# Kernel optimization log

Hardware: AMD Instinct MI355X
Metric: run time of the kernel (lower is better)

Reference implementation:

```python
import jax, jax.numpy as jnp
import numpy as np

N_NEIGHBORS = 3


def square_distance(src, dst):
    # src: [B,N,3], dst: [B,M,3] -> [B,N,M]
    d = -2.0 * jnp.einsum('bnc,bmc->bnm', src, dst)
    d = d + jnp.sum(src * src, axis=-1)[:, :, None]
    d = d + jnp.sum(dst * dst, axis=-1)[:, None, :]
    return d


def setup_inputs() -> dict:
    key = jax.random.key(0)
    k1, k2, k3 = jax.random.split(key, 3)
    B, N_q, N_k, C = 4, 8192, 2048, 128
    xyz_q = jax.random.normal(k1, (B, N_q, 3), dtype=jnp.float32)
    xyz_k = jax.random.normal(k2, (B, N_k, 3), dtype=jnp.float32)
    v_k = jax.random.normal(k3, (B, N_k, C), dtype=jnp.float32)
    return {"xyz_q": xyz_q, "xyz_k": xyz_k, "v_k": v_k}


def reference(xyz_q, xyz_k, v_k):
    # pairwise squared distances [B,N_q,N_k]
    sqrdists = square_distance(xyz_q, xyz_k)
    # kNN: smallest nsample distances per query
    neg_dist, idx = jax.lax.top_k(-sqrdists, N_NEIGHBORS)  # [B,N_q,k]
    dist_nearest = jnp.take_along_axis(sqrdists, idx, axis=2)
    dist_nearest = jnp.maximum(dist_nearest, 1e-10)
    weights = 1.0 / dist_nearest
    weights = weights / jnp.sum(weights, axis=-1, keepdims=True)
    # gather neighbor features: [B,N_q,k,C]
    grouped_v = jax.vmap(lambda v, i: v[i])(v_k, idx)
    # inverse-distance-weighted interpolation
    v_q = jnp.einsum('bnk,bnkc->bnc', weights, grouped_v)
    return v_q
```

## Files before the change

### kernel.cpp

```cpp
#include <hip/hip_runtime.h>
#include <cfloat>

#define BB 4
#define NQ 8192
#define NK 2048
#define CC 128
#define C4 (CC / 4)

#define QPB 64
#define SPLITS 16
#define KPS (NK / SPLITS)
#define NTHR (QPB * SPLITS)

__global__ __launch_bounds__(NTHR, 8) void fp_fused(
    const float*  __restrict__ xyz_q,
    const float*  __restrict__ xyz_k,
    const float4* __restrict__ vk,
    float4*       __restrict__ out)
{
    __shared__ float4 ks[NK];
    __shared__ unsigned long long rd[NTHR][4];
    __shared__ float sw[QPB][4];
    __shared__ int   si[QPB][4];

    const int b     = blockIdx.y;
    const int qbase = blockIdx.x * QPB;
    const int tid   = threadIdx.x;
    const int lane  = tid & 63;
    const int split = tid >> 6;
    const int q     = qbase + lane;

    {
        const float* kb = xyz_k + (size_t)b * NK * 3;
        #pragma unroll
        for (int i = tid; i < NK; i += NTHR) {
            ks[i] = make_float4(kb[i * 3 + 0], kb[i * 3 + 1], kb[i * 3 + 2], 0.0f);
        }
    }

    const float qx = xyz_q[(b * NQ + q) * 3 + 0];
    const float qy = xyz_q[(b * NQ + q) * 3 + 1];
    const float qz = xyz_q[(b * NQ + q) * 3 + 2];

    __syncthreads();

    const int kbeg = __builtin_amdgcn_readfirstlane(split * KPS);

    float u0 = FLT_MAX, u1 = FLT_MAX, u2 = FLT_MAX, u3 = FLT_MAX;

    #pragma unroll 8
    for (int j = 0; j < KPS; ++j) {
        float4 kk = ks[kbeg + j];
        float dx = qx - kk.x, dy = qy - kk.y, dz = qz - kk.z;
        float t = fmaf(dx, dx, fmaf(dy, dy, dz * dz));
        float p = __uint_as_float((__float_as_uint(t) & 0xFFFFFF80u) | (unsigned)j);
        u3 = __builtin_amdgcn_fmed3f(p, u2, u3);
        u2 = __builtin_amdgcn_fmed3f(p, u1, u2);
        u1 = __builtin_amdgcn_fmed3f(p, u0, u1);
        u0 = fminf(u0, p);
    }

    {
        float uu[4] = { u0, u1, u2, u3 };
        #pragma unroll
        for (int c = 0; c < 4; ++c) {
            int kidx = kbeg + (int)(__float_as_uint(uu[c]) & 0x7Fu);
            float4 ka = ks[kidx];
            double dx = (double)qx - (double)ka.x;
            double dy = (double)qy - (double)ka.y;
            double dz = (double)qz - (double)ka.z;
            double dd = dx * dx + dy * dy + dz * dz;
            unsigned long long pk =
                (((unsigned long long)__double_as_longlong(dd)) & ~0x7FFull)
                | (unsigned long long)kidx;
            rd[tid][c] = pk;
        }
    }
    __syncthreads();

    if (tid < QPB) {
        double m0 = DBL_MAX, m1 = DBL_MAX, m2 = DBL_MAX;
        #pragma unroll 4
        for (int s = 0; s < SPLITS; ++s) {
            #pragma unroll
            for (int c = 0; c < 4; ++c) {
                double x = __longlong_as_double((long long)rd[s * QPB + lane][c]);
                double a1 = fmax(x, m1), a0 = fmax(x, m0);
                m2 = fmin(m2, a1);
                m1 = fmin(m1, a0);
                m0 = fmin(m0, x);
            }
        }
        unsigned long long b0 = (unsigned long long)__double_as_longlong(m0);
        unsigned long long b1 = (unsigned long long)__double_as_longlong(m1);
        unsigned long long b2 = (unsigned long long)__double_as_longlong(m2);
        double e0 = __longlong_as_double((long long)(b0 & ~0x7FFull));
        double e1 = __longlong_as_double((long long)(b1 & ~0x7FFull));
        double e2 = __longlong_as_double((long long)(b2 & ~0x7FFull));
        e0 = fmax(e0, 1e-10);
        e1 = fmax(e1, 1e-10);
        e2 = fmax(e2, 1e-10);
        double w0 = 1.0 / e0, w1 = 1.0 / e1, w2 = 1.0 / e2;
        double s  = w0 + w1 + w2;
        sw[lane][0] = (float)(w0 / s);
        sw[lane][1] = (float)(w1 / s);
        sw[lane][2] = (float)(w2 / s);
        si[lane][0] = (int)(b0 & 0x7FFull);
        si[lane][1] = (int)(b1 & 0x7FFull);
        si[lane][2] = (int)(b2 & 0x7FFull);
    }
    __syncthreads();

    const float4* vb = vk + (size_t)b * NK * C4;
    float4* ob = out + ((size_t)b * NQ + qbase) * C4;
    #pragma unroll
    for (int r = 0; r < (QPB * C4) / NTHR; ++r) {
        int o  = r * NTHR + tid;
        int qq = o >> 5;
        int c4 = o & (C4 - 1);
        float w0 = sw[qq][0], w1 = sw[qq][1], w2 = sw[qq][2];
        int   j0 = si[qq][0], j1 = si[qq][1], j2 = si[qq][2];
        float4 v0 = vb[j0 * C4 + c4];
        float4 v1 = vb[j1 * C4 + c4];
        float4 v2 = vb[j2 * C4 + c4];
        float4 res;
        res.x = fmaf(w0, v0.x, fmaf(w1, v1.x, w2 * v2.x));
        res.y = fmaf(w0, v0.y, fmaf(w1, v1.y, w2 * v2.y));
        res.z = fmaf(w0, v0.z, fmaf(w1, v1.z, w2 * v2.z));
        res.w = fmaf(w0, v0.w, fmaf(w1, v1.w, w2 * v2.w));
        ob[o] = res;
    }
}

extern "C" void kernel_launch(void* const* d_in, const int* in_sizes, int n_in,
                              void* d_out, int out_size, void* d_ws, size_t ws_size,
                              hipStream_t stream)
{
    const float* xyz_q = (const float*)d_in[0];
    const float* xyz_k = (const float*)d_in[1];
    const float* v_k   = (const float*)d_in[2];

    fp_fused<<<dim3(NQ / QPB, BB), dim3(NTHR), 0, stream>>>(
        xyz_q, xyz_k, (const float4*)v_k, (float4*)d_out);
}
```

Measured before the change: 89.20 us.

## Stream keys via scalar loads from a prepacked global buffer instead of LDS

Adds a pre-pass kernel that packs key coordinates with their squared norm into float4 in the workspace. The main kernel drops the LDS key staging and its barrier, and reads 4 keys per iteration with wave-uniform s_load_dwordx16 into SGPRs. The distance is computed in expanded form (q^2 + k^2 - 2q·k, with a small offset added). This aims to remove LDS read traffic and cut per-key VALU work. The risks are a serialising lgkmcnt wait each iteration with unroll 1, an extra kernel launch, and the expanded-form distance reordering near-ties before the double-precision refinement.

Result: slower. 92.87 us (+4.1%).

```diff
diff --git a/kernel.cpp b/kernel.cpp
--- a/kernel.cpp
+++ b/kernel.cpp
@@ -12,13 +12,26 @@
 #define KPS (NK / SPLITS)
 #define NTHR (QPB * SPLITS)
 
-__global__ __launch_bounds__(NTHR, 8) void fp_fused(
+typedef float sfvec __attribute__((ext_vector_type(16)));
+
+__global__ __launch_bounds__(256) void pack_keys(
+    const float* __restrict__ xyz_k, float4* __restrict__ keys)
+{
+    int i = blockIdx.x * 256 + threadIdx.x;
+    if (i < BB * NK) {
+        float x = xyz_k[i * 3 + 0];
+        float y = xyz_k[i * 3 + 1];
+        float z = xyz_k[i * 3 + 2];
+        keys[i] = make_float4(x, y, z, fmaf(x, x, fmaf(y, y, z * z)));
+    }
+}
+
+__global__ __launch_bounds__(NTHR, 8) void fp_main(
     const float*  __restrict__ xyz_q,
-    const float*  __restrict__ xyz_k,
+    const float4* __restrict__ keys,
     const float4* __restrict__ vk,
     float4*       __restrict__ out)
 {
-    __shared__ float4 ks[NK];
     __shared__ unsigned long long rd[NTHR][4];
     __shared__ float sw[QPB][4];
     __shared__ int   si[QPB][4];
@@ -30,42 +43,46 @@
     const int split = tid >> 6;
     const int q     = qbase + lane;
 
-    {
-        const float* kb = xyz_k + (size_t)b * NK * 3;
+    const float qx = xyz_q[(b * NQ + q) * 3 + 0];
+    const float qy = xyz_q[(b * NQ + q) * 3 + 1];
+    const float qz = xyz_q[(b * NQ + q) * 3 + 2];
+    const float qq = fmaf(qx, qx, fmaf(qy, qy, qz * qz)) + 1.0e-3f;
+    const float ax = -2.0f * qx, ay = -2.0f * qy, az = -2.0f * qz;
+
+    const int kbeg = __builtin_amdgcn_readfirstlane(split * KPS);
+    const sfvec* kp4 = (const sfvec*)(keys + (size_t)b * NK + kbeg);
+
+    float u0 = FLT_MAX, u1 = FLT_MAX, u2 = FLT_MAX, u3 = FLT_MAX;
+
+    #pragma unroll 1
+    for (int jb = 0; jb < KPS / 4; ++jb) {
+        const sfvec* addr = kp4 + jb;
+        sfvec kk;
+        asm("s_load_dwordx16 %0, %1, 0x0" : "=s"(kk) : "s"(addr));
+        asm("s_waitcnt lgkmcnt(0)" : "+s"(kk));
         #pragma unroll
-        for (int i = tid; i < NK; i += NTHR) {
-            ks[i] = make_float4(kb[i * 3 + 0], kb[i * 3 + 1], kb[i * 3 + 2], 0.0f);
+        for (int c = 0; c < 4; ++c) {
+            float kx = kk[c * 4 + 0];
+            float ky = kk[c * 4 + 1];
+            float kz = kk[c * 4 + 2];
+            float kw = kk[c * 4 + 3];
+            float t = fmaf(ax, kx, fmaf(ay, ky, fmaf(az, kz, qq))) + kw;
+            float p = __uint_as_float((__float_as_uint(t) & 0xFFFFFF80u)
+                                      | (unsigned)(jb * 4 + c));
+            u3 = __builtin_amdgcn_fmed3f(p, u2, u3);
+            u2 = __builtin_amdgcn_fmed3f(p, u1, u2);
+            u1 = __builtin_amdgcn_fmed3f(p, u0, u1);
+            u0 = fminf(u0, p);
         }
     }
 
-    const float qx = xyz_q[(b * NQ + q) * 3 + 0];
-    const float qy = xyz_q[(b * NQ + q) * 3 + 1];
-    const float qz = xyz_q[(b * NQ + q) * 3 + 2];
-
-    __syncthreads();
-
-    const int kbeg = __builtin_amdgcn_readfirstlane(split * KPS);
-
-    float u0 = FLT_MAX, u1 = FLT_MAX, u2 = FLT_MAX, u3 = FLT_MAX;
-
-    #pragma unroll 8
-    for (int j = 0; j < KPS; ++j) {
-        float4 kk = ks[kbeg + j];
-        float dx = qx - kk.x, dy = qy - kk.y, dz = qz - kk.z;
-        float t = fmaf(dx, dx, fmaf(dy, dy, dz * dz));
-        float p = __uint_as_float((__float_as_uint(t) & 0xFFFFFF80u) | (unsigned)j);
-        u3 = __builtin_amdgcn_fmed3f(p, u2, u3);
-        u2 = __builtin_amdgcn_fmed3f(p, u1, u2);
-        u1 = __builtin_amdgcn_fmed3f(p, u0, u1);
-        u0 = fminf(u0, p);
-    }
-
     {
+        const float4* kg = keys + (size_t)b * NK;
         float uu[4] = { u0, u1, u2, u3 };
         #pragma unroll
         for (int c = 0; c < 4; ++c) {
             int kidx = kbeg + (int)(__float_as_uint(uu[c]) & 0x7Fu);
-            float4 ka = ks[kidx];
+            float4 ka = kg[kidx];
             double dx = (double)qx - (double)ka.x;
             double dy = (double)qy - (double)ka.y;
             double dz = (double)qz - (double)ka.z;
@@ -116,10 +133,10 @@
     #pragma unroll
     for (int r = 0; r < (QPB * C4) / NTHR; ++r) {
         int o  = r * NTHR + tid;
-        int qq = o >> 5;
+        int qq2 = o >> 5;
         int c4 = o & (C4 - 1);
-        float w0 = sw[qq][0], w1 = sw[qq][1], w2 = sw[qq][2];
-        int   j0 = si[qq][0], j1 = si[qq][1], j2 = si[qq][2];
+        float w0 = sw[qq2][0], w1 = sw[qq2][1], w2 = sw[qq2][2];
+        int   j0 = si[qq2][0], j1 = si[qq2][1], j2 = si[qq2][2];
         float4 v0 = vb[j0 * C4 + c4];
         float4 v1 = vb[j1 * C4 + c4];
         float4 v2 = vb[j2 * C4 + c4];
@@ -140,6 +157,9 @@
     const float* xyz_k = (const float*)d_in[1];
     const float* v_k   = (const float*)d_in[2];
 
-    fp_fused<<<dim3(NQ / QPB, BB), dim3(NTHR), 0, stream>>>(
-        xyz_q, xyz_k, (const float4*)v_k, (float4*)d_out);
+    float4* keys = (float4*)d_ws;
+
+    pack_keys<<<dim3((BB * NK + 255) / 256), dim3(256), 0, stream>>>(xyz_k, keys);
+    fp_main<<<dim3(NQ / QPB, BB), dim3(NTHR), 0, stream>>>(
+        xyz_q, keys, (const float4*)v_k, (float4*)d_out);
 }
```

## Expand distance algebraically, process four queries per thread, prepack keys

Applied to the files above, without the earlier changes.

A new pre-kernel packs the key coordinates plus their squared norm into float4 in workspace. The main kernel computes distance as q·(-2k)+|q|²+|k|², which cuts per-pair arithmetic. Each thread now handles four queries, so one shared-memory key load is reused across them and the thread count drops to 256. The fp32 scan keeps top-4 per split with an 11-bit index packed into the low mantissa bits. Merging keeps top-8 candidates that are re-ranked in double precision, which adds a second launch and a more approximate fp32 pre-filter in exchange.

New measurement: 90.23 us. About the same (+1.1%).

```diff
diff --git a/kernel.cpp b/kernel.cpp
--- a/kernel.cpp
+++ b/kernel.cpp
@@ -10,90 +10,137 @@
 #define QPB 64
 #define SPLITS 16
 #define KPS (NK / SPLITS)
-#define NTHR (QPB * SPLITS)
+#define QPT 4
+#define NTHR (QPB * SPLITS / QPT)
+#define RD_ROW 68
 
-__global__ __launch_bounds__(NTHR, 8) void fp_fused(
+static __device__ __forceinline__ float fmed3(float a, float b, float c) {
+    return __builtin_amdgcn_fmed3f(a, b, c);
+}
+
+__global__ __launch_bounds__(256) void pack_keys(
+    const float* __restrict__ xyz_k, float4* __restrict__ keys)
+{
+    int i = blockIdx.x * 256 + threadIdx.x;
+    if (i < BB * NK) {
+        float x = xyz_k[i * 3 + 0];
+        float y = xyz_k[i * 3 + 1];
+        float z = xyz_k[i * 3 + 2];
+        keys[i] = make_float4(x, y, z, fmaf(x, x, fmaf(y, y, z * z)));
+    }
+}
+
+__global__ __launch_bounds__(NTHR, 2) void fp_main(
     const float*  __restrict__ xyz_q,
-    const float*  __restrict__ xyz_k,
+    const float4* __restrict__ keys,
     const float4* __restrict__ vk,
     float4*       __restrict__ out)
 {
-    __shared__ float4 ks[NK];
-    __shared__ unsigned long long rd[NTHR][4];
-    __shared__ float sw[QPB][4];
-    __shared__ int   si[QPB][4];
+    __shared__ float4  ks[NK];
+    __shared__ unsigned rd[QPB][RD_ROW];
+    __shared__ float   sw[QPB][4];
+    __shared__ int     si[QPB][4];
 
     const int b     = blockIdx.y;
     const int qbase = blockIdx.x * QPB;
     const int tid   = threadIdx.x;
-    const int lane  = tid & 63;
-    const int split = tid >> 6;
-    const int q     = qbase + lane;
+    const int split = tid >> 4;
+    const int g     = tid & 15;
 
-    {
-        const float* kb = xyz_k + (size_t)b * NK * 3;
-        #pragma unroll
-        for (int i = tid; i < NK; i += NTHR) {
-            ks[i] = make_float4(kb[i * 3 + 0], kb[i * 3 + 1], kb[i * 3 + 2], 0.0f);
-        }
+    #pragma unroll
+    for (int i = tid; i < NK; i += NTHR) ks[i] = keys[(size_t)b * NK + i];
+
+    float ax[QPT], ay[QPT], az[QPT], qb_[QPT];
+    #pragma unroll
+    for (int qi = 0; qi < QPT; ++qi) {
+        int q = qbase + g + 16 * qi;
+        float qx = xyz_q[(b * NQ + q) * 3 + 0];
+        float qy = xyz_q[(b * NQ + q) * 3 + 1];
+        float qz = xyz_q[(b * NQ + q) * 3 + 2];
+        ax[qi] = -2.0f * qx; ay[qi] = -2.0f * qy; az[qi] = -2.0f * qz;
+        qb_[qi] = fmaf(qx, qx, fmaf(qy, qy, qz * qz)) + 1.0e-3f;
     }
-
-    const float qx = xyz_q[(b * NQ + q) * 3 + 0];
-    const float qy = xyz_q[(b * NQ + q) * 3 + 1];
-    const float qz = xyz_q[(b * NQ + q) * 3 + 2];
-
     __syncthreads();
 
-    const int kbeg = __builtin_amdgcn_readfirstlane(split * KPS);
+    const int kbeg = split * KPS;
 
-    float u0 = FLT_MAX, u1 = FLT_MAX, u2 = FLT_MAX, u3 = FLT_MAX;
+    float u[QPT][4];
+    #pragma unroll
+    for (int qi = 0; qi < QPT; ++qi)
+        u[qi][0] = u[qi][1] = u[qi][2] = u[qi][3] = FLT_MAX;
 
     #pragma unroll 8
     for (int j = 0; j < KPS; ++j) {
         float4 kk = ks[kbeg + j];
-        float dx = qx - kk.x, dy = qy - kk.y, dz = qz - kk.z;
-        float t = fmaf(dx, dx, fmaf(dy, dy, dz * dz));
-        float p = __uint_as_float((__float_as_uint(t) & 0xFFFFFF80u) | (unsigned)j);
-        u3 = __builtin_amdgcn_fmed3f(p, u2, u3);
-        u2 = __builtin_amdgcn_fmed3f(p, u1, u2);
-        u1 = __builtin_amdgcn_fmed3f(p, u0, u1);
-        u0 = fminf(u0, p);
+        unsigned kidx = (unsigned)(kbeg + j);
+        #pragma unroll
+        for (int qi = 0; qi < QPT; ++qi) {
+            float t = fmaf(ax[qi], kk.x,
+                      fmaf(ay[qi], kk.y,
+                      fmaf(az[qi], kk.z, qb_[qi]))) + kk.w;
+            float p = __uint_as_float((__float_as_uint(t) & 0xFFFFF800u) | kidx);
+            u[qi][3] = fmed3(p, u[qi][2], u[qi][3]);
+            u[qi][2] = fmed3(p, u[qi][1], u[qi][2]);
+            u[qi][1] = fmed3(p, u[qi][0], u[qi][1]);
+            u[qi][0] = fminf(u[qi][0], p);
+        }
     }
 
-    {
-        float uu[4] = { u0, u1, u2, u3 };
-        #pragma unroll
-        for (int c = 0; c < 4; ++c) {
-            int kidx = kbeg + (int)(__float_as_uint(uu[c]) & 0x7Fu);
-            float4 ka = ks[kidx];
-            double dx = (double)qx - (double)ka.x;
-            double dy = (double)qy - (double)ka.y;
-            double dz = (double)qz - (double)ka.z;
-            double dd = dx * dx + dy * dy + dz * dz;
-            unsigned long long pk =
-                (((unsigned long long)__double_as_longlong(dd)) & ~0x7FFull)
-                | (unsigned long long)kidx;
-            rd[tid][c] = pk;
-        }
+    #pragma unroll
+    for (int qi = 0; qi < QPT; ++qi) {
+        int ql = g + 16 * qi;
+        uint4 v = make_uint4(__float_as_uint(u[qi][0]), __float_as_uint(u[qi][1]),
+                             __float_as_uint(u[qi][2]), __float_as_uint(u[qi][3]));
+        *(uint4*)&rd[ql][split * 4] = v;
     }
     __syncthreads();
 
     if (tid < QPB) {
-        double m0 = DBL_MAX, m1 = DBL_MAX, m2 = DBL_MAX;
+        const int ql = tid;
+        float m[8];
+        #pragma unroll
+        for (int c = 0; c < 8; ++c) m[c] = FLT_MAX;
         #pragma unroll 4
-        for (int s = 0; s < SPLITS; ++s) {
+        for (int i = 0; i < SPLITS; ++i) {
+            uint4 v = *(const uint4*)&rd[ql][i * 4];
+            unsigned vv[4] = { v.x, v.y, v.z, v.w };
             #pragma unroll
             for (int c = 0; c < 4; ++c) {
-                double x = __longlong_as_double((long long)rd[s * QPB + lane][c]);
-                double a1 = fmax(x, m1), a0 = fmax(x, m0);
-                m2 = fmin(m2, a1);
-                m1 = fmin(m1, a0);
-                m0 = fmin(m0, x);
+                float p = __uint_as_float(vv[c]);
+                m[7] = fmed3(p, m[6], m[7]);
+                m[6] = fmed3(p, m[5], m[6]);
+                m[5] = fmed3(p, m[4], m[5]);
+                m[4] = fmed3(p, m[3], m[4]);
+                m[3] = fmed3(p, m[2], m[3]);
+                m[2] = fmed3(p, m[1], m[2]);
+                m[1] = fmed3(p, m[0], m[1]);
+                m[0] = fminf(m[0], p);
             }
         }
-        unsigned long long b0 = (unsigned long long)__double_as_longlong(m0);
-        unsigned long long b1 = (unsigned long long)__double_as_longlong(m1);
-        unsigned long long b2 = (unsigned long long)__double_as_longlong(m2);
+        int q = qbase + ql;
+        double qx = (double)xyz_q[(b * NQ + q) * 3 + 0];
+        double qy = (double)xyz_q[(b * NQ + q) * 3 + 1];
+        double qz = (double)xyz_q[(b * NQ + q) * 3 + 2];
+        double M0 = DBL_MAX, M1 = DBL_MAX, M2 = DBL_MAX;
+        #pragma unroll
+        for (int c = 0; c < 8; ++c) {
+            unsigned ki = __float_as_uint(m[c]) & 0x7FFu;
+            float4 ka = ks[ki];
+            double dx = qx - (double)ka.x;
+            double dy = qy - (double)ka.y;
+            double dz = qz - (double)ka.z;
+            double dd = dx * dx + dy * dy + dz * dz;
+            double x = __longlong_as_double(
+                (long long)((((unsigned long long)__double_as_longlong(dd)) & ~0x7FFull)
+                            | (unsigned long long)ki));
+            double a1 = fmax(x, M1), a0 = fmax(x, M0);
+            M2 = fmin(M2, a1);
+            M1 = fmin(M1, a0);
+            M0 = fmin(M0, x);
+        }
+        unsigned long long b0 = (unsigned long long)__double_as_longlong(M0);
+        unsigned long long b1 = (unsigned long long)__double_as_longlong(M1);
+        unsigned long long b2 = (unsigned long long)__double_as_longlong(M2);
         double e0 = __longlong_as_double((long long)(b0 & ~0x7FFull));
         double e1 = __longlong_as_double((long long)(b1 & ~0x7FFull));
         double e2 = __longlong_as_double((long long)(b2 & ~0x7FFull));
@@ -102,12 +149,12 @@
         e2 = fmax(e2, 1e-10);
         double w0 = 1.0 / e0, w1 = 1.0 / e1, w2 = 1.0 / e2;
         double s  = w0 + w1 + w2;
-        sw[lane][0] = (float)(w0 / s);
-        sw[lane][1] = (float)(w1 / s);
-        sw[lane][2] = (float)(w2 / s);
-        si[lane][0] = (int)(b0 & 0x7FFull);
-        si[lane][1] = (int)(b1 & 0x7FFull);
-        si[lane][2] = (int)(b2 & 0x7FFull);
+        sw[ql][0] = (float)(w0 / s);
+        sw[ql][1] = (float)(w1 / s);
+        sw[ql][2] = (float)(w2 / s);
+        si[ql][0] = (int)(b0 & 0x7FFull);
+        si[ql][1] = (int)(b1 & 0x7FFull);
+        si[ql][2] = (int)(b2 & 0x7FFull);
     }
     __syncthreads();
 
@@ -140,6 +187,9 @@
     const float* xyz_k = (const float*)d_in[1];
     const float* v_k   = (const float*)d_in[2];
 
-    fp_fused<<<dim3(NQ / QPB, BB), dim3(NTHR), 0, stream>>>(
-        xyz_q, xyz_k, (const float4*)v_k, (float4*)d_out);
+    float4* keys = (float4*)d_ws;
+
+    pack_keys<<<dim3((BB * NK + 255) / 256), dim3(256), 0, stream>>>(xyz_k, keys);
+    fp_main<<<dim3(NQ / QPB, BB), dim3(NTHR), 0, stream>>>(
+        xyz_q, keys, (const float4*)v_k, (float4*)d_out);
 }
```
